# Kernel tuning notes

Hardware: AMD Instinct MI355X
Metric: run time of the kernel (lower is better)

Reference implementation:

```python
import jax, jax.numpy as jnp
import numpy as np

N = 10000
E = 320000
NDIM_IN = 128
EDIM = 128
NDIM_OUT = 128
HID = 152  # size_embedding
NCLS = 15  # nbclasses


def _lin(k, out_f, in_f, scale=0.05):
    kw, kb = jax.random.split(k)
    W = jax.random.normal(kw, (out_f, in_f), dtype=jnp.float32) * scale
    b = jax.random.normal(kb, (out_f,), dtype=jnp.float32) * scale
    return W, b


def setup_inputs() -> dict:
    key = jax.random.key(0)
    ks = jax.random.split(key, 12)
    nfeats = jax.random.normal(ks[0], (N, 1, NDIM_IN), dtype=jnp.float32)
    efeats = jax.random.normal(ks[1], (E, 1, EDIM), dtype=jnp.float32)
    src = jax.random.randint(ks[2], (E,), 0, N)
    dst = jax.random.randint(ks[3], (E,), 0, N)
    # SAGE layer 1: msg (ndim_in+edim -> 152), apply (ndim_in+152 -> 152)
    Wm1, bm1 = _lin(ks[4], HID, NDIM_IN + EDIM)
    Wa1, ba1 = _lin(ks[5], HID, NDIM_IN + HID)
    # layer 2: msg (152+edim -> 152), apply (152+152 -> 152)
    Wm2, bm2 = _lin(ks[6], HID, HID + EDIM)
    Wa2, ba2 = _lin(ks[7], HID, HID + HID)
    # layer 3: msg (152+edim -> ndim_out), apply (152+ndim_out -> ndim_out)
    Wm3, bm3 = _lin(ks[8], NDIM_OUT, HID + EDIM)
    Wa3, ba3 = _lin(ks[9], NDIM_OUT, HID + NDIM_OUT)
    # edge predictor: Linear(2*ndim_out -> nbclasses)
    Wp, bp = _lin(ks[10], NCLS, 2 * NDIM_OUT)
    return {"nfeats": nfeats, "efeats": efeats, "src": src, "dst": dst,
            "Wm1": Wm1, "bm1": bm1, "Wa1": Wa1, "ba1": ba1,
            "Wm2": Wm2, "bm2": bm2, "Wa2": Wa2, "ba2": ba2,
            "Wm3": Wm3, "bm3": bm3, "Wa3": Wa3, "ba3": ba3,
            "Wp": Wp, "bp": bp}


def _sage_layer(h, e, src, dst, Wm, bm, Wa, ba):
    # h: [N,1,din]  e: [E,1,edim]
    msg = jnp.concatenate([h[src], e], axis=-1) @ Wm.T + bm  # [E,1,dout]
    agg = jax.ops.segment_sum(msg, dst, num_segments=N)       # [N,1,dout]
    deg = jax.ops.segment_sum(jnp.ones((E,), dtype=h.dtype), dst, num_segments=N)
    h_neigh = agg / jnp.maximum(deg, 1.0)[:, None, None]      # mean; 0 for isolated nodes
    return jax.nn.relu(jnp.concatenate([h, h_neigh], axis=-1) @ Wa.T + ba)


def reference(nfeats, efeats, src, dst,
              Wm1, bm1, Wa1, ba1, Wm2, bm2, Wa2, ba2,
              Wm3, bm3, Wa3, ba3, Wp, bp):
    h = _sage_layer(nfeats, efeats, src, dst, Wm1, bm1, Wa1, ba1)
    h = _sage_layer(h, efeats, src, dst, Wm2, bm2, Wa2, ba2)  # dropout is identity in eval
    h = _sage_layer(h, efeats, src, dst, Wm3, bm3, Wa3, ba3)
    h = h.sum(axis=1)  # [N, ndim_out]
    v = jnp.concatenate([h[src], h[dst]], axis=1)  # [E, 2*ndim_out]
    return v @ Wp.T + bp  # [E, nbclasses]
```

## Files before the change

### kernel.cpp

```cpp
#include <hip/hip_runtime.h>
#include <hip/hip_bf16.h>
#include <cstdint>


static inline int cdiv(int a, int b) { return (a + b - 1) / b; }

#define NN 10000
#define NE 320000
#define MTB 313
#define MD 192

typedef __attribute__((ext_vector_type(8))) short bf16x8;
typedef __attribute__((ext_vector_type(4))) float f32x4;

__device__ __forceinline__ ushort f2bf(float x) {
  union { float f; unsigned u; } c; c.f = x;
  unsigned r = c.u + 0x7FFFu + ((c.u >> 16) & 1u);
  return (ushort)(r >> 16);
}
__device__ __forceinline__ float bf2f(unsigned h) {
  union { unsigned u; float f; } c; c.u = h << 16;
  return c.f;
}
__device__ __forceinline__ f32x4 mfma3(bf16x8 ah, bf16x8 al, bf16x8 bh, bf16x8 bl,
                                       f32x4 acc) {
  acc = __builtin_amdgcn_mfma_f32_16x16x32_bf16(ah, bh, acc, 0, 0, 0);
  acc = __builtin_amdgcn_mfma_f32_16x16x32_bf16(al, bh, acc, 0, 0, 0);
  acc = __builtin_amdgcn_mfma_f32_16x16x32_bf16(ah, bl, acc, 0, 0, 0);
  return acc;
}
__device__ __forceinline__ void ld32frag(const float* p, bf16x8& h, bf16x8& l) {
  float4 x0 = *(const float4*)p;
  float4 x1 = *(const float4*)(p + 4);
  float v[8] = {x0.x, x0.y, x0.z, x0.w, x1.x, x1.y, x1.z, x1.w};
#pragma unroll
  for (int j = 0; j < 8; ++j) {
    ushort hh = f2bf(v[j]);
    h[j] = (short)hh;
    l[j] = (short)f2bf(v[j] - bf2f(hh));
  }
}
__device__ __forceinline__ void wpack1(ushort* lds, int base, int KT, int row,
                                       int k, float v) {
  int idx0 = base + ((k >> 5) * 4 + ((k >> 3) & 3)) * 256 + row * 8 + (k & 7);
  ushort h = f2bf(v);
  lds[idx0] = h;
  lds[idx0 + KT * 1024] = f2bf(v - bf2f(h));
}
__device__ __forceinline__ bf16x8 rfrag(const ushort* lds, int base, int KT,
                                        int plane, int kt, int lane, int mh) {
  int idx = base + ((plane * KT + kt) * 4 + (lane >> 4)) * 256 +
            ((lane & 15) + 16 * mh) * 8;
  return *reinterpret_cast<const bf16x8*>(&lds[idx]);
}

__global__ __launch_bounds__(256) void k_bucket(const int* __restrict__ src,
                                                const int* __restrict__ dst,
                                                int* __restrict__ fill,
                                                int2* __restrict__ bk) {
  int e = blockIdx.x * 256 + threadIdx.x;
  if (e < NE) {
    int d = dst[e];
    int pos = atomicAdd(&fill[d], 1);
    if (pos < MD) bk[d * MD + pos] = make_int2(e, src[e]);
  }
}

struct WDesc {
  const float* W; ushort* hi; ushort* lo;
  int dout, KA, KApad, KB, Korig, NG16, KT, pred;
};
struct PrepArgs {
  WDesc d[7];
  int* fill;
};

__global__ __launch_bounds__(256) void k_prep(PrepArgs P) {
  const int y = blockIdx.y;
  if (y == 7) {
    int i = blockIdx.x * 256 + threadIdx.x;
    if (i < NN) P.fill[i] = 0;
    return;
  }
  const WDesc d = P.d[y];
  int tid = blockIdx.x * 256 + threadIdx.x;
  if (tid >= d.KT * d.NG16 * 64) return;
  int lane = tid & 63;
  int g = (tid >> 6) % d.NG16;
  int t = (tid >> 6) / d.NG16;
  int col = g * 16 + (lane & 15);
  int kbase = t * 32 + ((lane >> 4) * 8);
  size_t o = (size_t)tid * 8;
#pragma unroll
  for (int j = 0; j < 8; ++j) {
    int kk = kbase + j;
    float w = 0.f;
    if (!d.pred) {
      if (col < d.dout) {
        if (kk < d.KApad) { if (kk < d.KA) w = d.W[(size_t)col * d.Korig + kk]; }
        else { int kb = kk - d.KApad; if (kb < d.KB) w = d.W[(size_t)col * d.Korig + d.KA + kb]; }
      }
    } else {
      if (col < 15) w = d.W[(size_t)col * 256 + kk];
      else if (col < 30) w = d.W[(size_t)(col - 15) * 256 + 128 + kk];
    }
    ushort h = f2bf(w);
    d.hi[o + j] = h;
    d.lo[o + j] = f2bf(w - bf2f(h));
  }
}

__global__ __launch_bounds__(64) void k_eaggproj(
    const float* __restrict__ efeats, const int2* __restrict__ bk,
    const int* __restrict__ fill, const float* __restrict__ nfeats,
    const ushort* __restrict__ Wm1h, const ushort* __restrict__ Wm1l,
    ushort* __restrict__ ehi, ushort* __restrict__ elo,
    float* __restrict__ deg, ushort* __restrict__ ph1) {
  const int lane = threadIdx.x;
  if (blockIdx.x < NN) {
    const int d = blockIdx.x;
    const int half = lane >> 5, cl = lane & 31;
    const int cntd = fill[d];
    const int n = min(cntd, MD);
    const int s = d * MD, t = s + n;
    float4 acc[8];
#pragma unroll
    for (int u = 0; u < 8; ++u) acc[u] = make_float4(0.f, 0.f, 0.f, 0.f);
    int j = s;
    for (; j + 15 < t; j += 16) {
#pragma unroll
      for (int u = 0; u < 8; ++u) {
        int e0 = bk[j + 2 * u + half].x;
        float4 v = *(const float4*)(efeats + (size_t)e0 * 128 + cl * 4);
        acc[u].x += v.x; acc[u].y += v.y; acc[u].z += v.z; acc[u].w += v.w;
      }
    }
    for (; j + 1 < t; j += 2) {
      int e0 = bk[j + half].x;
      float4 v = *(const float4*)(efeats + (size_t)e0 * 128 + cl * 4);
      acc[0].x += v.x; acc[0].y += v.y; acc[0].z += v.z; acc[0].w += v.w;
    }
    if (j < t && half == 0) {
      int e0 = bk[j].x;
      float4 v = *(const float4*)(efeats + (size_t)e0 * 128 + cl * 4);
      acc[0].x += v.x; acc[0].y += v.y; acc[0].z += v.z; acc[0].w += v.w;
    }
#pragma unroll
    for (int u = 4; u > 0; u >>= 1)
#pragma unroll
      for (int w = 0; w < u; ++w) {
        acc[w].x += acc[w + u].x; acc[w].y += acc[w + u].y;
        acc[w].z += acc[w + u].z; acc[w].w += acc[w + u].w;
      }
    float4 sm = acc[0];
    sm.x += __shfl_xor(sm.x, 32);
    sm.y += __shfl_xor(sm.y, 32);
    sm.z += __shfl_xor(sm.z, 32);
    sm.w += __shfl_xor(sm.w, 32);
    if (lane < 32) {
      size_t o = (size_t)d * 128 + cl * 4;
      ushort h0 = f2bf(sm.x), h1 = f2bf(sm.y), h2 = f2bf(sm.z), h3 = f2bf(sm.w);
      uint2 uh, ul;
      uh.x = (unsigned)h0 | ((unsigned)h1 << 16);
      uh.y = (unsigned)h2 | ((unsigned)h3 << 16);
      ul.x = (unsigned)f2bf(sm.x - bf2f(h0)) | ((unsigned)f2bf(sm.y - bf2f(h1)) << 16);
      ul.y = (unsigned)f2bf(sm.z - bf2f(h2)) | ((unsigned)f2bf(sm.w - bf2f(h3)) << 16);
      *(uint2*)(ehi + o) = uh;
      *(uint2*)(elo + o) = ul;
    }
    if (lane == 0) deg[d] = (float)cntd;
    return;
  }
  const int p = blockIdx.x - NN;
  const int ng0 = (p % 5) * 2;
  const int row0 = (p / 5) * 32;
  const int rA = lane & 15, kl = (lane >> 4) * 8, colL = lane & 15;
  const int r0 = min(row0 + rA, NN - 1), r1 = min(row0 + 16 + rA, NN - 1);
  f32x4 a00 = {0.f, 0.f, 0.f, 0.f}, a01 = {0.f, 0.f, 0.f, 0.f};
  f32x4 a10 = {0.f, 0.f, 0.f, 0.f}, a11 = {0.f, 0.f, 0.f, 0.f};
#pragma unroll
  for (int kt = 0; kt < 4; ++kt) {
    bf16x8 a0h, a0l, a1h, a1l;
    ld32frag(nfeats + (size_t)r0 * 128 + kt * 32 + kl, a0h, a0l);
    ld32frag(nfeats + (size_t)r1 * 128 + kt * 32 + kl, a1h, a1l);
    size_t wb = ((size_t)(kt * 10 + ng0) * 64 + lane) * 8;
    bf16x8 b0h = *(const bf16x8*)(Wm1h + wb), b0l = *(const bf16x8*)(Wm1l + wb);
    bf16x8 b1h = *(const bf16x8*)(Wm1h + wb + 512), b1l = *(const bf16x8*)(Wm1l + wb + 512);
    a00 = mfma3(a0h, a0l, b0h, b0l, a00);
    a01 = mfma3(a0h, a0l, b1h, b1l, a01);
    a10 = mfma3(a1h, a1l, b0h, b0l, a10);
    a11 = mfma3(a1h, a1l, b1h, b1l, a11);
  }
#pragma unroll
  for (int ms = 0; ms < 2; ++ms) {
    const f32x4 aN0 = ms ? a10 : a00;
    const f32x4 aN1 = ms ? a11 : a01;
#pragma unroll
    for (int reg = 0; reg < 4; ++reg) {
      int row = row0 + ms * 16 + (lane >> 4) * 4 + reg;
      if (row >= NN) continue;
#pragma unroll
      for (int ns = 0; ns < 2; ++ns) {
        int col = (ng0 + ns) * 16 + colL;
        float v = ns ? aN1[reg] : aN0[reg];
        ph1[(size_t)row * 160 + col] = f2bf(col < 152 ? v : 0.f);
      }
    }
  }
}

template <int WP>
__global__ __launch_bounds__(64) void k_gath(const ushort* __restrict__ ph,
                                             const int2* __restrict__ bk,
                                             const int* __restrict__ fill,
                                             float* __restrict__ gsum) {
  constexpr int QUADS = WP / 4;
  const int d = blockIdx.x, lane = threadIdx.x;
  const int n = min(fill[d], MD);
  const int s = d * MD, t = s + n;
  float4 a0 = {0.f, 0.f, 0.f, 0.f}, a1 = a0, a2 = a0, a3 = a0;
  int j = s;
  for (; j + 3 < t; j += 4) {
    int s0 = bk[j].y, s1 = bk[j + 1].y, s2 = bk[j + 2].y, s3 = bk[j + 3].y;
    if (lane < QUADS) {
      uint2 u0 = *(const uint2*)(ph + (size_t)s0 * WP + 4 * lane);
      uint2 u1 = *(const uint2*)(ph + (size_t)s1 * WP + 4 * lane);
      uint2 u2 = *(const uint2*)(ph + (size_t)s2 * WP + 4 * lane);
      uint2 u3 = *(const uint2*)(ph + (size_t)s3 * WP + 4 * lane);
      a0.x += bf2f(u0.x & 0xffffu); a0.y += bf2f(u0.x >> 16);
      a0.z += bf2f(u0.y & 0xffffu); a0.w += bf2f(u0.y >> 16);
      a1.x += bf2f(u1.x & 0xffffu); a1.y += bf2f(u1.x >> 16);
      a1.z += bf2f(u1.y & 0xffffu); a1.w += bf2f(u1.y >> 16);
      a2.x += bf2f(u2.x & 0xffffu); a2.y += bf2f(u2.x >> 16);
      a2.z += bf2f(u2.y & 0xffffu); a2.w += bf2f(u2.y >> 16);
      a3.x += bf2f(u3.x & 0xffffu); a3.y += bf2f(u3.x >> 16);
      a3.z += bf2f(u3.y & 0xffffu); a3.w += bf2f(u3.y >> 16);
    }
  }
  for (; j < t; ++j) {
    int s0 = bk[j].y;
    if (lane < QUADS) {
      uint2 u0 = *(const uint2*)(ph + (size_t)s0 * WP + 4 * lane);
      a0.x += bf2f(u0.x & 0xffffu); a0.y += bf2f(u0.x >> 16);
      a0.z += bf2f(u0.y & 0xffffu); a0.w += bf2f(u0.y >> 16);
    }
  }
  if (lane < QUADS) {
    float4 r;
    r.x = (a0.x + a1.x) + (a2.x + a3.x);
    r.y = (a0.y + a1.y) + (a2.y + a3.y);
    r.z = (a0.z + a1.z) + (a2.z + a3.z);
    r.w = (a0.w + a1.w) + (a2.w + a3.w);
    *(float4*)(gsum + (size_t)d * WP + 4 * lane) = r;
  }
}

template <int KTH, int KTNM, int NGA, int NGP, bool PRED, bool A32>
__global__ __launch_bounds__(NGA * 32) void k_applyproj(
    const ushort* __restrict__ Ahi, const ushort* __restrict__ Alo,
    const float* __restrict__ Af, const float* __restrict__ gsum,
    const ushort* __restrict__ eah, const ushort* __restrict__ eal,
    const ushort* __restrict__ Wmeh, const ushort* __restrict__ Wmel,
    const float* __restrict__ bm, const float* __restrict__ deg,
    int NG16M, int dout_m,
    const ushort* __restrict__ Wah, const ushort* __restrict__ Wal,
    const float* __restrict__ ba,
    ushort* __restrict__ Yhi, ushort* __restrict__ Ylo,
    const ushort* __restrict__ Wnh, const ushort* __restrict__ Wnl,
    ushort* __restrict__ phout, float* __restrict__ hsd,
    int dout_a, int dout_p) {
  constexpr int KTO = NGA / 2;
  constexpr int OSTR = KTO * 32;
  constexpr int SA = KTH * 32;
  constexpr int WPAD = KTNM * 32;
  constexpr int OSTR2 = NGP * 16;
  constexpr int BASE_OUT = 2 * KTNM * 1024;
  __shared__ ushort lds[BASE_OUT + 2 * KTO * 1024];
  const int tid = threadIdx.x;
  const int wid = tid >> 6, lane = tid & 63;
  const int rA = lane & 15, kl = (lane >> 4) * 8, colL = lane & 15;
  const int q = lane >> 4;
  const int row0 = blockIdx.x * 32;
  const int r0 = min(row0 + rA, NN - 1), r1 = min(row0 + 16 + rA, NN - 1);
  if (wid < KTNM) {
    const int ng0 = wid * 2;
    f32x4 a00 = {0.f, 0.f, 0.f, 0.f}, a01 = {0.f, 0.f, 0.f, 0.f};
    f32x4 a10 = {0.f, 0.f, 0.f, 0.f}, a11 = {0.f, 0.f, 0.f, 0.f};
#pragma unroll
    for (int kt = 0; kt < 4; ++kt) {
      size_t o0 = (size_t)r0 * 128 + kt * 32 + kl;
      size_t o1 = (size_t)r1 * 128 + kt * 32 + kl;
      bf16x8 a0h = *(const bf16x8*)(eah + o0), a0l = *(const bf16x8*)(eal + o0);
      bf16x8 a1h = *(const bf16x8*)(eah + o1), a1l = *(const bf16x8*)(eal + o1);
      size_t wb = ((size_t)(kt * NG16M + ng0) * 64 + lane) * 8;
      bf16x8 b0h = *(const bf16x8*)(Wmeh + wb), b0l = *(const bf16x8*)(Wmel + wb);
      bf16x8 b1h = *(const bf16x8*)(Wmeh + wb + 512), b1l = *(const bf16x8*)(Wmel + wb + 512);
      a00 = mfma3(a0h, a0l, b0h, b0l, a00);
      a01 = mfma3(a0h, a0l, b1h, b1l, a01);
      a10 = mfma3(a1h, a1l, b0h, b0l, a10);
      a11 = mfma3(a1h, a1l, b1h, b1l, a11);
    }
#pragma unroll
    for (int ms = 0; ms < 2; ++ms) {
      const f32x4 aN0 = ms ? a10 : a00;
      const f32x4 aN1 = ms ? a11 : a01;
#pragma unroll
      for (int reg = 0; reg < 4; ++reg) {
        int rloc = ms * 16 + (lane >> 4) * 4 + reg;
        int row = row0 + rloc;
        float dg = (row < NN) ? deg[row] : 0.f;
        float inv = 1.f / fmaxf(dg, 1.f);
#pragma unroll
        for (int ns = 0; ns < 2; ++ns) {
          int col = (ng0 + ns) * 16 + colL;
          float acc = ns ? aN1[reg] : aN0[reg];
          float y = 0.f;
          if (col < dout_m && row < NN)
            y = (gsum[(size_t)row * WPAD + col] + acc + dg * bm[col]) * inv;
          wpack1(lds, 0, KTNM, rloc, col, y);
        }
      }
    }
  }
  __syncthreads();
  if (wid < NGA / 2) {
    const int ng0 = wid * 2;
    f32x4 a00 = {0.f, 0.f, 0.f, 0.f}, a01 = {0.f, 0.f, 0.f, 0.f};
    f32x4 a10 = {0.f, 0.f, 0.f, 0.f}, a11 = {0.f, 0.f, 0.f, 0.f};
#pragma unroll
    for (int kt = 0; kt < KTH + KTNM; ++kt) {
      bf16x8 a0h, a0l, a1h, a1l;
      if (kt < KTH) {
        if constexpr (A32) {
          ld32frag(Af + (size_t)r0 * SA + kt * 32 + kl, a0h, a0l);
          ld32frag(Af + (size_t)r1 * SA + kt * 32 + kl, a1h, a1l);
        } else {
          size_t o0 = (size_t)r0 * SA + kt * 32 + kl;
          size_t o1 = (size_t)r1 * SA + kt * 32 + kl;
          a0h = *(const bf16x8*)(Ahi + o0); a0l = *(const bf16x8*)(Alo + o0);
          a1h = *(const bf16x8*)(Ahi + o1); a1l = *(const bf16x8*)(Alo + o1);
        }
      } else {
        const int rkt = kt - KTH;
        a0h = rfrag(lds, 0, KTNM, 0, rkt, lane, 0);
        a0l = rfrag(lds, 0, KTNM, 1, rkt, lane, 0);
        a1h = rfrag(lds, 0, KTNM, 0, rkt, lane, 1);
        a1l = rfrag(lds, 0, KTNM, 1, rkt, lane, 1);
      }
      size_t wb = ((size_t)(kt * NGA + ng0) * 64 + lane) * 8;
      bf16x8 b0h = *(const bf16x8*)(Wah + wb), b0l = *(const bf16x8*)(Wal + wb);
      bf16x8 b1h = *(const bf16x8*)(Wah + wb + 512), b1l = *(const bf16x8*)(Wal + wb + 512);
      a00 = mfma3(a0h, a0l, b0h, b0l, a00);
      a01 = mfma3(a0h, a0l, b1h, b1l, a01);
      a10 = mfma3(a1h, a1l, b0h, b0l, a10);
      a11 = mfma3(a1h, a1l, b1h, b1l, a11);
    }
#pragma unroll
    for (int ms = 0; ms < 2; ++ms) {
      const f32x4 aN0 = ms ? a10 : a00;
      const f32x4 aN1 = ms ? a11 : a01;
#pragma unroll
      for (int reg = 0; reg < 4; ++reg) {
        int rloc = ms * 16 + (lane >> 4) * 4 + reg;
        int row = row0 + rloc;
#pragma unroll
        for (int ns = 0; ns < 2; ++ns) {
          int col = (ng0 + ns) * 16 + colL;
          float v = ns ? aN1[reg] : aN0[reg];
          float y = (col < dout_a) ? fmaxf(v + ba[col], 0.f) : 0.f;
          ushort h = f2bf(y), l = f2bf(y - bf2f(h));
          int idx = BASE_OUT + ((col >> 5) * 4 + ((col >> 3) & 3)) * 256 + rloc * 8 + (col & 7);
          lds[idx] = h;
          lds[idx + KTO * 1024] = l;
          if constexpr (!PRED) {
            if (row < NN) {
              Yhi[(size_t)row * OSTR + col] = h;
              Ylo[(size_t)row * OSTR + col] = l;
            }
          }
        }
      }
    }
  }
  __syncthreads();
  if (wid < NGP / 2) {
    const int ng0 = wid * 2;
    f32x4 a00 = {0.f, 0.f, 0.f, 0.f}, a01 = {0.f, 0.f, 0.f, 0.f};
    f32x4 a10 = {0.f, 0.f, 0.f, 0.f}, a11 = {0.f, 0.f, 0.f, 0.f};
#pragma unroll
    for (int kt = 0; kt < KTO; ++kt) {
      int b0 = BASE_OUT + (kt * 4 + q) * 256;
      int b1 = BASE_OUT + ((KTO + kt) * 4 + q) * 256;
      bf16x8 a0h = *(const bf16x8*)(lds + b0 + rA * 8);
      bf16x8 a1h = *(const bf16x8*)(lds + b0 + (rA + 16) * 8);
      bf16x8 a0l = *(const bf16x8*)(lds + b1 + rA * 8);
      bf16x8 a1l = *(const bf16x8*)(lds + b1 + (rA + 16) * 8);
      size_t wb = ((size_t)(kt * NGP + ng0) * 64 + lane) * 8;
      bf16x8 b0h = *(const bf16x8*)(Wnh + wb), b0l = *(const bf16x8*)(Wnl + wb);
      bf16x8 b1h = *(const bf16x8*)(Wnh + wb + 512), b1l = *(const bf16x8*)(Wnl + wb + 512);
      a00 = mfma3(a0h, a0l, b0h, b0l, a00);
      a01 = mfma3(a0h, a0l, b1h, b1l, a01);
      a10 = mfma3(a1h, a1l, b0h, b0l, a10);
      a11 = mfma3(a1h, a1l, b1h, b1l, a11);
    }
#pragma unroll
    for (int ms = 0; ms < 2; ++ms) {
      const f32x4 aN0 = ms ? a10 : a00;
      const f32x4 aN1 = ms ? a11 : a01;
#pragma unroll
      for (int reg = 0; reg < 4; ++reg) {
        int row = row0 + ms * 16 + (lane >> 4) * 4 + reg;
        if (row >= NN) continue;
#pragma unroll
        for (int ns = 0; ns < 2; ++ns) {
          int col = (ng0 + ns) * 16 + colL;
          float v = ns ? aN1[reg] : aN0[reg];
          if constexpr (PRED)
            hsd[(size_t)row * 32 + col] = v;
          else
            phout[(size_t)row * OSTR2 + col] = f2bf(col < dout_p ? v : 0.f);
        }
      }
    }
  }
}

__global__ __launch_bounds__(256) void k_edge_out(const int* __restrict__ src,
                                                  const int* __restrict__ dst,
                                                  const float* __restrict__ hsd,
                                                  const float* __restrict__ bp,
                                                  float* __restrict__ out) {
  int i = blockIdx.x * 256 + threadIdx.x;
  if (i >= NE * 15) return;
  int e = i / 15, c = i - e * 15;
  out[i] = hsd[(size_t)src[e] * 32 + c] + hsd[(size_t)dst[e] * 32 + 15 + c] + bp[c];
}

extern "C" void kernel_launch(void* const* d_in, const int* in_sizes, int n_in,
                              void* d_out, int out_size, void* d_ws, size_t ws_size,
                              hipStream_t stream) {
  const float* nfeats = (const float*)d_in[0];
  const float* efeats = (const float*)d_in[1];
  const int* src = (const int*)d_in[2];
  const int* dst = (const int*)d_in[3];
  const float* Wm1 = (const float*)d_in[4];
  const float* bm1 = (const float*)d_in[5];
  const float* Wa1 = (const float*)d_in[6];
  const float* ba1 = (const float*)d_in[7];
  const float* Wm2 = (const float*)d_in[8];
  const float* bm2 = (const float*)d_in[9];
  const float* Wa2 = (const float*)d_in[10];
  const float* ba2 = (const float*)d_in[11];
  const float* Wm3 = (const float*)d_in[12];
  const float* bm3 = (const float*)d_in[13];
  const float* Wa3 = (const float*)d_in[14];
  const float* ba3 = (const float*)d_in[15];
  const float* Wp = (const float*)d_in[16];
  const float* bp = (const float*)d_in[17];
  float* out = (float*)d_out;

  char* base = (char*)d_ws;
  size_t woff = 0;
  auto alloc = [&](size_t bytes) -> void* {
    void* p = base + woff;
    woff += (bytes + 255) & ~(size_t)255;
    return p;
  };
  int* fill = (int*)alloc((size_t)NN * 4);
  int2* bk = (int2*)alloc((size_t)NN * MD * 8);
  float* deg = (float*)alloc((size_t)NN * 4);
  auto aplane = [&](int w) { return (ushort*)alloc((size_t)NN * w * 2); };
  ushort* eah = aplane(128); ushort* eal = aplane(128);
  ushort* h1h = aplane(160); ushort* h1l = aplane(160);
  ushort* h2h = aplane(160); ushort* h2l = aplane(160);
  ushort* ph1 = aplane(160); ushort* ph2 = aplane(160);
  float* gsum = (float*)alloc((size_t)NN * 160 * 4);
  float* hsd = (float*)alloc((size_t)NN * 32 * 4);
  auto wpk = [&](int kt, int ng) { return (ushort*)alloc((size_t)kt * ng * 512 * 2); };
  ushort* Wm1h = wpk(8, 10);  ushort* Wm1l = wpk(8, 10);
  ushort* Wa1h = wpk(9, 10);  ushort* Wa1l = wpk(9, 10);
  ushort* Wm2h = wpk(9, 10);  ushort* Wm2l = wpk(9, 10);
  ushort* Wa2h = wpk(10, 10); ushort* Wa2l = wpk(10, 10);
  ushort* Wm3h = wpk(9, 8);   ushort* Wm3l = wpk(9, 8);
  ushort* Wa3h = wpk(9, 8);   ushort* Wa3l = wpk(9, 8);
  ushort* Wpph = wpk(4, 2);   ushort* Wppl = wpk(4, 2);

  PrepArgs pa;
  pa.d[0] = {Wm1, Wm1h, Wm1l, 152, 128, 128, 128, 256, 10, 8, 0};
  pa.d[1] = {Wa1, Wa1h, Wa1l, 152, 128, 128, 152, 280, 10, 9, 0};
  pa.d[2] = {Wm2, Wm2h, Wm2l, 152, 152, 160, 128, 280, 10, 9, 0};
  pa.d[3] = {Wa2, Wa2h, Wa2l, 152, 152, 160, 152, 304, 10, 10, 0};
  pa.d[4] = {Wm3, Wm3h, Wm3l, 128, 152, 160, 128, 280, 8, 9, 0};
  pa.d[5] = {Wa3, Wa3h, Wa3l, 128, 152, 160, 128, 280, 8, 9, 0};
  pa.d[6] = {Wp, Wpph, Wppl, 32, 128, 128, 0, 256, 2, 4, 1};
  pa.fill = fill;
  k_prep<<<dim3(40, 8), 256, 0, stream>>>(pa);

  k_bucket<<<cdiv(NE, 256), 256, 0, stream>>>(src, dst, fill, bk);

  k_eaggproj<<<NN + 5 * MTB, 64, 0, stream>>>(
      efeats, bk, fill, nfeats, Wm1h, Wm1l, eah, eal, deg, ph1);

  k_gath<160><<<NN, 64, 0, stream>>>(ph1, bk, fill, gsum);
  k_applyproj<4, 5, 10, 10, false, true><<<MTB, 320, 0, stream>>>(
      nullptr, nullptr, nfeats, gsum, eah, eal,
      Wm1h + (size_t)4 * 10 * 512, Wm1l + (size_t)4 * 10 * 512, bm1, deg, 10, 152,
      Wa1h, Wa1l, ba1, h1h, h1l, Wm2h, Wm2l, ph2, nullptr, 152, 152);
  k_gath<160><<<NN, 64, 0, stream>>>(ph2, bk, fill, gsum);
  k_applyproj<5, 5, 10, 8, false, false><<<MTB, 320, 0, stream>>>(
      h1h, h1l, nullptr, gsum, eah, eal,
      Wm2h + (size_t)5 * 10 * 512, Wm2l + (size_t)5 * 10 * 512, bm2, deg, 10, 152,
      Wa2h, Wa2l, ba2, h2h, h2l, Wm3h, Wm3l, ph1, nullptr, 152, 128);
  k_gath<128><<<NN, 64, 0, stream>>>(ph1, bk, fill, gsum);
  k_applyproj<5, 4, 8, 2, true, false><<<MTB, 256, 0, stream>>>(
      h2h, h2l, nullptr, gsum, eah, eal,
      Wm3h + (size_t)5 * 8 * 512, Wm3l + (size_t)5 * 8 * 512, bm3, deg, 8, 128,
      Wa3h, Wa3l, ba3, nullptr, nullptr, Wpph, Wppl, nullptr, hsd, 128, 32);

  k_edge_out<<<cdiv(NE * 15, 256), 256, 0, stream>>>(src, dst, hsd, bp, out);
}
```

Baseline: 219.4 us.

## Hoist edge-aggregate message projections for all layers into first gather kernel

The per-layer projection of aggregated edge features through the edge part of each message weight is moved out of the three apply kernels. All three projections are now computed by extra blocks appended to the first gather launch, which writes them to new fp32 buffers. The apply kernels then only read gsum plus the precomputed projection with vectorized float4 loads and pack them with a 4-wide LDS store. This takes MFMA work off the critical path of layers 2 and 3 and lets it overlap with the layer-1 gather, at the cost of extra global buffers and extra memory traffic to read them back.

```diff
diff --git a/kernel.cpp b/kernel.cpp
--- a/kernel.cpp
+++ b/kernel.cpp
@@ -40,12 +40,20 @@
     l[j] = (short)f2bf(v[j] - bf2f(hh));
   }
 }
-__device__ __forceinline__ void wpack1(ushort* lds, int base, int KT, int row,
-                                       int k, float v) {
-  int idx0 = base + ((k >> 5) * 4 + ((k >> 3) & 3)) * 256 + row * 8 + (k & 7);
-  ushort h = f2bf(v);
-  lds[idx0] = h;
-  lds[idx0 + KT * 1024] = f2bf(v - bf2f(h));
+__device__ __forceinline__ void wpack4(ushort* lds, int base, int KT, int row,
+                                       int k0, float4 v) {
+  int idx0 = base + ((k0 >> 5) * 4 + ((k0 >> 3) & 3)) * 256 + row * 8 + (k0 & 7);
+  int idx1 = idx0 + KT * 1024;
+  ushort h0 = f2bf(v.x), h1 = f2bf(v.y), h2 = f2bf(v.z), h3 = f2bf(v.w);
+  uint2 uh, ul;
+  uh.x = (unsigned)h0 | ((unsigned)h1 << 16);
+  uh.y = (unsigned)h2 | ((unsigned)h3 << 16);
+  ushort l0 = f2bf(v.x - bf2f(h0)), l1 = f2bf(v.y - bf2f(h1));
+  ushort l2 = f2bf(v.z - bf2f(h2)), l3 = f2bf(v.w - bf2f(h3));
+  ul.x = (unsigned)l0 | ((unsigned)l1 << 16);
+  ul.y = (unsigned)l2 | ((unsigned)l3 << 16);
+  *reinterpret_cast<uint2*>(&lds[idx0]) = uh;
+  *reinterpret_cast<uint2*>(&lds[idx1]) = ul;
 }
 __device__ __forceinline__ bf16x8 rfrag(const ushort* lds, int base, int KT,
                                         int plane, int kt, int lane, int mh) {
@@ -209,49 +217,105 @@
   }
 }
 
-template <int WP>
-__global__ __launch_bounds__(64) void k_gath(const ushort* __restrict__ ph,
-                                             const int2* __restrict__ bk,
-                                             const int* __restrict__ fill,
-                                             float* __restrict__ gsum) {
-  constexpr int QUADS = WP / 4;
-  const int d = blockIdx.x, lane = threadIdx.x;
-  const int n = min(fill[d], MD);
-  const int s = d * MD, t = s + n;
-  float4 a0 = {0.f, 0.f, 0.f, 0.f}, a1 = a0, a2 = a0, a3 = a0;
-  int j = s;
-  for (; j + 3 < t; j += 4) {
-    int s0 = bk[j].y, s1 = bk[j + 1].y, s2 = bk[j + 2].y, s3 = bk[j + 3].y;
+template <int WP, bool PE>
+__global__ __launch_bounds__(64) void k_gath(
+    const ushort* __restrict__ ph, const int2* __restrict__ bk,
+    const int* __restrict__ fill, float* __restrict__ gsum,
+    const ushort* __restrict__ eah, const ushort* __restrict__ eal,
+    const ushort* __restrict__ pW1h, const ushort* __restrict__ pW1l,
+    const ushort* __restrict__ pW2h, const ushort* __restrict__ pW2l,
+    const ushort* __restrict__ pW3h, const ushort* __restrict__ pW3l,
+    const float* __restrict__ bm1, const float* __restrict__ bm2,
+    const float* __restrict__ bm3, const float* __restrict__ deg,
+    float* __restrict__ pe1, float* __restrict__ pe2, float* __restrict__ pe3) {
+  const int lane = threadIdx.x;
+  if (!PE || blockIdx.x < NN) {
+    constexpr int QUADS = WP / 4;
+    const int d = blockIdx.x;
+    const int n = min(fill[d], MD);
+    const int s = d * MD, t = s + n;
+    float4 a0 = {0.f, 0.f, 0.f, 0.f}, a1 = a0, a2 = a0, a3 = a0;
+    int j = s;
+    for (; j + 3 < t; j += 4) {
+      int s0 = bk[j].y, s1 = bk[j + 1].y, s2 = bk[j + 2].y, s3 = bk[j + 3].y;
+      if (lane < QUADS) {
+        uint2 u0 = *(const uint2*)(ph + (size_t)s0 * WP + 4 * lane);
+        uint2 u1 = *(const uint2*)(ph + (size_t)s1 * WP + 4 * lane);
+        uint2 u2 = *(const uint2*)(ph + (size_t)s2 * WP + 4 * lane);
+        uint2 u3 = *(const uint2*)(ph + (size_t)s3 * WP + 4 * lane);
+        a0.x += bf2f(u0.x & 0xffffu); a0.y += bf2f(u0.x >> 16);
+        a0.z += bf2f(u0.y & 0xffffu); a0.w += bf2f(u0.y >> 16);
+        a1.x += bf2f(u1.x & 0xffffu); a1.y += bf2f(u1.x >> 16);
+        a1.z += bf2f(u1.y & 0xffffu); a1.w += bf2f(u1.y >> 16);
+        a2.x += bf2f(u2.x & 0xffffu); a2.y += bf2f(u2.x >> 16);
+        a2.z += bf2f(u2.y & 0xffffu); a2.w += bf2f(u2.y >> 16);
+        a3.x += bf2f(u3.x & 0xffffu); a3.y += bf2f(u3.x >> 16);
+        a3.z += bf2f(u3.y & 0xffffu); a3.w += bf2f(u3.y >> 16);
+      }
+    }
+    for (; j < t; ++j) {
+      int s0 = bk[j].y;
+      if (lane < QUADS) {
+        uint2 u0 = *(const uint2*)(ph + (size_t)s0 * WP + 4 * lane);
+        a0.x += bf2f(u0.x & 0xffffu); a0.y += bf2f(u0.x >> 16);
+        a0.z += bf2f(u0.y & 0xffffu); a0.w += bf2f(u0.y >> 16);
+      }
+    }
     if (lane < QUADS) {
-      uint2 u0 = *(const uint2*)(ph + (size_t)s0 * WP + 4 * lane);
-      uint2 u1 = *(const uint2*)(ph + (size_t)s1 * WP + 4 * lane);
-      uint2 u2 = *(const uint2*)(ph + (size_t)s2 * WP + 4 * lane);
-      uint2 u3 = *(const uint2*)(ph + (size_t)s3 * WP + 4 * lane);
-      a0.x += bf2f(u0.x & 0xffffu); a0.y += bf2f(u0.x >> 16);
-      a0.z += bf2f(u0.y & 0xffffu); a0.w += bf2f(u0.y >> 16);
-      a1.x += bf2f(u1.x & 0xffffu); a1.y += bf2f(u1.x >> 16);
-      a1.z += bf2f(u1.y & 0xffffu); a1.w += bf2f(u1.y >> 16);
-      a2.x += bf2f(u2.x & 0xffffu); a2.y += bf2f(u2.x >> 16);
-      a2.z += bf2f(u2.y & 0xffffu); a2.w += bf2f(u2.y >> 16);
-      a3.x += bf2f(u3.x & 0xffffu); a3.y += bf2f(u3.x >> 16);
-      a3.z += bf2f(u3.y & 0xffffu); a3.w += bf2f(u3.y >> 16);
-    }
-  }
-  for (; j < t; ++j) {
-    int s0 = bk[j].y;
-    if (lane < QUADS) {
-      uint2 u0 = *(const uint2*)(ph + (size_t)s0 * WP + 4 * lane);
-      a0.x += bf2f(u0.x & 0xffffu); a0.y += bf2f(u0.x >> 16);
-      a0.z += bf2f(u0.y & 0xffffu); a0.w += bf2f(u0.y >> 16);
-    }
-  }
-  if (lane < QUADS) {
-    float4 r;
-    r.x = (a0.x + a1.x) + (a2.x + a3.x);
-    r.y = (a0.y + a1.y) + (a2.y + a3.y);
-    r.z = (a0.z + a1.z) + (a2.z + a3.z);
-    r.w = (a0.w + a1.w) + (a2.w + a3.w);
-    *(float4*)(gsum + (size_t)d * WP + 4 * lane) = r;
+      float4 r;
+      r.x = (a0.x + a1.x) + (a2.x + a3.x);
+      r.y = (a0.y + a1.y) + (a2.y + a3.y);
+      r.z = (a0.z + a1.z) + (a2.z + a3.z);
+      r.w = (a0.w + a1.w) + (a2.w + a3.w);
+      *(float4*)(gsum + (size_t)d * WP + 4 * lane) = r;
+    }
+    return;
+  }
+  const int b = blockIdx.x - NN;
+  const int jid = b % 14;
+  const int row0 = (b / 14) * 32;
+  const ushort *Wh, *Wl;
+  const float* bm;
+  float* pe;
+  int NG16 = 10, ng0, WPAD = 160, dout = 152;
+  if (jid < 5) { Wh = pW1h; Wl = pW1l; bm = bm1; pe = pe1; ng0 = jid * 2; }
+  else if (jid < 10) { Wh = pW2h; Wl = pW2l; bm = bm2; pe = pe2; ng0 = (jid - 5) * 2; }
+  else { Wh = pW3h; Wl = pW3l; bm = bm3; pe = pe3; ng0 = (jid - 10) * 2;
+         NG16 = 8; WPAD = 128; dout = 128; }
+  const int rA = lane & 15, kl = (lane >> 4) * 8, colL = lane & 15;
+  const int r0 = min(row0 + rA, NN - 1), r1 = min(row0 + 16 + rA, NN - 1);
+  f32x4 a00 = {0.f, 0.f, 0.f, 0.f}, a01 = {0.f, 0.f, 0.f, 0.f};
+  f32x4 a10 = {0.f, 0.f, 0.f, 0.f}, a11 = {0.f, 0.f, 0.f, 0.f};
+#pragma unroll
+  for (int kt = 0; kt < 4; ++kt) {
+    size_t o0 = (size_t)r0 * 128 + kt * 32 + kl;
+    size_t o1 = (size_t)r1 * 128 + kt * 32 + kl;
+    bf16x8 a0h = *(const bf16x8*)(eah + o0), a0l = *(const bf16x8*)(eal + o0);
+    bf16x8 a1h = *(const bf16x8*)(eah + o1), a1l = *(const bf16x8*)(eal + o1);
+    size_t wb = ((size_t)(kt * NG16 + ng0) * 64 + lane) * 8;
+    bf16x8 b0h = *(const bf16x8*)(Wh + wb), b0l = *(const bf16x8*)(Wl + wb);
+    bf16x8 b1h = *(const bf16x8*)(Wh + wb + 512), b1l = *(const bf16x8*)(Wl + wb + 512);
+    a00 = mfma3(a0h, a0l, b0h, b0l, a00);
+    a01 = mfma3(a0h, a0l, b1h, b1l, a01);
+    a10 = mfma3(a1h, a1l, b0h, b0l, a10);
+    a11 = mfma3(a1h, a1l, b1h, b1l, a11);
+  }
+#pragma unroll
+  for (int ms = 0; ms < 2; ++ms) {
+    const f32x4 aN0 = ms ? a10 : a00;
+    const f32x4 aN1 = ms ? a11 : a01;
+#pragma unroll
+    for (int reg = 0; reg < 4; ++reg) {
+      int row = row0 + ms * 16 + (lane >> 4) * 4 + reg;
+      if (row >= NN) continue;
+      float dg = deg[row];
+#pragma unroll
+      for (int ns = 0; ns < 2; ++ns) {
+        int col = (ng0 + ns) * 16 + colL;
+        float v = ns ? aN1[reg] : aN0[reg];
+        pe[(size_t)row * WPAD + col] = (col < dout) ? v + dg * bm[col] : 0.f;
+      }
+    }
   }
 }
 
@@ -259,10 +323,7 @@
 __global__ __launch_bounds__(NGA * 32) void k_applyproj(
     const ushort* __restrict__ Ahi, const ushort* __restrict__ Alo,
     const float* __restrict__ Af, const float* __restrict__ gsum,
-    const ushort* __restrict__ eah, const ushort* __restrict__ eal,
-    const ushort* __restrict__ Wmeh, const ushort* __restrict__ Wmel,
-    const float* __restrict__ bm, const float* __restrict__ deg,
-    int NG16M, int dout_m,
+    const float* __restrict__ pe, const float* __restrict__ deg,
     const ushort* __restrict__ Wah, const ushort* __restrict__ Wal,
     const float* __restrict__ ba,
     ushort* __restrict__ Yhi, ushort* __restrict__ Ylo,
@@ -282,44 +343,24 @@
   const int q = lane >> 4;
   const int row0 = blockIdx.x * 32;
   const int r0 = min(row0 + rA, NN - 1), r1 = min(row0 + 16 + rA, NN - 1);
-  if (wid < KTNM) {
-    const int ng0 = wid * 2;
-    f32x4 a00 = {0.f, 0.f, 0.f, 0.f}, a01 = {0.f, 0.f, 0.f, 0.f};
-    f32x4 a10 = {0.f, 0.f, 0.f, 0.f}, a11 = {0.f, 0.f, 0.f, 0.f};
-#pragma unroll
-    for (int kt = 0; kt < 4; ++kt) {
-      size_t o0 = (size_t)r0 * 128 + kt * 32 + kl;
-      size_t o1 = (size_t)r1 * 128 + kt * 32 + kl;
-      bf16x8 a0h = *(const bf16x8*)(eah + o0), a0l = *(const bf16x8*)(eal + o0);
-      bf16x8 a1h = *(const bf16x8*)(eah + o1), a1l = *(const bf16x8*)(eal + o1);
-      size_t wb = ((size_t)(kt * NG16M + ng0) * 64 + lane) * 8;
-      bf16x8 b0h = *(const bf16x8*)(Wmeh + wb), b0l = *(const bf16x8*)(Wmel + wb);
-      bf16x8 b1h = *(const bf16x8*)(Wmeh + wb + 512), b1l = *(const bf16x8*)(Wmel + wb + 512);
-      a00 = mfma3(a0h, a0l, b0h, b0l, a00);
-      a01 = mfma3(a0h, a0l, b1h, b1l, a01);
-      a10 = mfma3(a1h, a1l, b0h, b0l, a10);
-      a11 = mfma3(a1h, a1l, b1h, b1l, a11);
-    }
-#pragma unroll
-    for (int ms = 0; ms < 2; ++ms) {
-      const f32x4 aN0 = ms ? a10 : a00;
-      const f32x4 aN1 = ms ? a11 : a01;
-#pragma unroll
-      for (int reg = 0; reg < 4; ++reg) {
-        int rloc = ms * 16 + (lane >> 4) * 4 + reg;
-        int row = row0 + rloc;
-        float dg = (row < NN) ? deg[row] : 0.f;
-        float inv = 1.f / fmaxf(dg, 1.f);
-#pragma unroll
-        for (int ns = 0; ns < 2; ++ns) {
-          int col = (ng0 + ns) * 16 + colL;
-          float acc = ns ? aN1[reg] : aN0[reg];
-          float y = 0.f;
-          if (col < dout_m && row < NN)
-            y = (gsum[(size_t)row * WPAD + col] + acc + dg * bm[col]) * inv;
-          wpack1(lds, 0, KTNM, rloc, col, y);
-        }
-      }
+  {
+    constexpr int NT = NGA * 32;
+    constexpr int TASKS = 32 * (WPAD / 4);
+    for (int task = tid; task < TASKS; task += NT) {
+      int row = task / (WPAD / 4);
+      int k0 = (task % (WPAD / 4)) * 4;
+      int grow = row0 + row;
+      float4 v = {0.f, 0.f, 0.f, 0.f};
+      if (grow < NN) {
+        float4 g = *(const float4*)(gsum + (size_t)grow * WPAD + k0);
+        float4 p = *(const float4*)(pe + (size_t)grow * WPAD + k0);
+        float inv = 1.f / fmaxf(deg[grow], 1.f);
+        v.x = (g.x + p.x) * inv;
+        v.y = (g.y + p.y) * inv;
+        v.z = (g.z + p.z) * inv;
+        v.w = (g.w + p.w) * inv;
+      }
+      wpack4(lds, 0, KTNM, row, k0, v);
     }
   }
   __syncthreads();
@@ -475,6 +516,9 @@
   ushort* h2h = aplane(160); ushort* h2l = aplane(160);
   ushort* ph1 = aplane(160); ushort* ph2 = aplane(160);
   float* gsum = (float*)alloc((size_t)NN * 160 * 4);
+  float* pe1 = (float*)alloc((size_t)NN * 160 * 4);
+  float* pe2 = (float*)alloc((size_t)NN * 160 * 4);
+  float* pe3 = (float*)alloc((size_t)NN * 128 * 4);
   float* hsd = (float*)alloc((size_t)NN * 32 * 4);
   auto wpk = [&](int kt, int ng) { return (ushort*)alloc((size_t)kt * ng * 512 * 2); };
   ushort* Wm1h = wpk(8, 10);  ushort* Wm1l = wpk(8, 10);
@@ -501,21 +545,31 @@
   k_eaggproj<<<NN + 5 * MTB, 64, 0, stream>>>(
       efeats, bk, fill, nfeats, Wm1h, Wm1l, eah, eal, deg, ph1);
 
-  k_gath<160><<<NN, 64, 0, stream>>>(ph1, bk, fill, gsum);
+  const ushort* pW1h = Wm1h + (size_t)4 * 10 * 512;
+  const ushort* pW1l = Wm1l + (size_t)4 * 10 * 512;
+  const ushort* pW2h = Wm2h + (size_t)5 * 10 * 512;
+  const ushort* pW2l = Wm2l + (size_t)5 * 10 * 512;
+  const ushort* pW3h = Wm3h + (size_t)5 * 8 * 512;
+  const ushort* pW3l = Wm3l + (size_t)5 * 8 * 512;
+
+  k_gath<160, true><<<NN + 14 * MTB, 64, 0, stream>>>(
+      ph1, bk, fill, gsum, eah, eal, pW1h, pW1l, pW2h, pW2l, pW3h, pW3l,
+      bm1, bm2, bm3, deg, pe1, pe2, pe3);
   k_applyproj<4, 5, 10, 10, false, true><<<MTB, 320, 0, stream>>>(
-      nullptr, nullptr, nfeats, gsum, eah, eal,
-      Wm1h + (size_t)4 * 10 * 512, Wm1l + (size_t)4 * 10 * 512, bm1, deg, 10, 152,
-      Wa1h, Wa1l, ba1, h1h, h1l, Wm2h, Wm2l, ph2, nullptr, 152, 152);
-  k_gath<160><<<NN, 64, 0, stream>>>(ph2, bk, fill, gsum);
+      nullptr, nullptr, nfeats, gsum, pe1, deg, Wa1h, Wa1l, ba1,
+      h1h, h1l, Wm2h, Wm2l, ph2, nullptr, 152, 152);
+  k_gath<160, false><<<NN, 64, 0, stream>>>(
+      ph2, bk, fill, gsum, nullptr, nullptr, nullptr, nullptr, nullptr, nullptr,
+      nullptr, nullptr, nullptr, nullptr, nullptr, deg, nullptr, nullptr, nullptr);
   k_applyproj<5, 5, 10, 8, false, false><<<MTB, 320, 0, stream>>>(
-      h1h, h1l, nullptr, gsum, eah, eal,
-      Wm2h + (size_t)5 * 10 * 512, Wm2l + (size_t)5 * 10 * 512, bm2, deg, 10, 152,
-      Wa2h, Wa2l, ba2, h2h, h2l, Wm3h, Wm3l, ph1, nullptr, 152, 128);
-  k_gath<128><<<NN, 64, 0, stream>>>(ph1, bk, fill, gsum);
+      h1h, h1l, nullptr, gsum, pe2, deg, Wa2h, Wa2l, ba2,
+      h2h, h2l, Wm3h, Wm3l, ph1, nullptr, 152, 128);
+  k_gath<128, false><<<NN, 64, 0, stream>>>(
+      ph1, bk, fill, gsum, nullptr, nullptr, nullptr, nullptr, nullptr, nullptr,
+      nullptr, nullptr, nullptr, nullptr, nullptr, deg, nullptr, nullptr, nullptr);
   k_applyproj<5, 4, 8, 2, true, false><<<MTB, 256, 0, stream>>>(
-      h2h, h2l, nullptr, gsum, eah, eal,
-      Wm3h + (size_t)5 * 8 * 512, Wm3l + (size_t)5 * 8 * 512, bm3, deg, 8, 128,
-      Wa3h, Wa3l, ba3, nullptr, nullptr, Wpph, Wppl, nullptr, hsd, 128, 32);
+      h2h, h2l, nullptr, gsum, pe3, deg, Wa3h, Wa3l, ba3,
+      nullptr, nullptr, Wpph, Wppl, nullptr, hsd, 128, 32);
 
   k_edge_out<<<cdiv(NE * 15, 256), 256, 0, stream>>>(src, dst, hsd, bp, out);
 }
```

Measured after the change: 201.6 us (median of 2 runs). -8.1%, faster.
